# Kernel tuning notes

Hardware: AMD Instinct MI355X
Metric: run time of the kernel (lower is better)

The kernel has to match this reference:

```python
import jax, jax.numpy as jnp
import numpy as np

POS_RATIO = 0.5
EPS = 1e-6


def setup_inputs() -> dict:
    key = jax.random.key(0)
    k1, k2, k3, k4 = jax.random.split(key, 4)
    N, C, D, H, W = 8, 256, 8, 16, 16
    q = jax.random.normal(k1, (N, C, D, H, W), dtype=jnp.float32)
    k = jax.random.normal(k2, (N, C, D, H, W), dtype=jnp.float32)
    # coords: (x0, y0, z0, x1, y1, z1) with lower-right > upper-left
    uq = jax.random.uniform(k3, (N, 3), dtype=jnp.float32) * 0.5
    uk = jax.random.uniform(k4, (N, 3), dtype=jnp.float32) * 0.5
    coord_q = jnp.concatenate([uq, uq + 0.5], axis=1)
    coord_k = jnp.concatenate([uk, uk + 0.5], axis=1)
    return {"q": q, "k": k, "coord_q": coord_q, "coord_k": coord_k}


def _centers(coord, D, H, W):
    """Per-batch voxel-center coordinates. coord: [N,6]. Returns cx, cy, cz each [N, D*H*W], plus bin diag [N]."""
    bw = (coord[:, 3] - coord[:, 0]) / W  # [N]
    bh = (coord[:, 4] - coord[:, 1]) / H
    bd = (coord[:, 5] - coord[:, 2]) / D
    gz, gy, gx = jnp.meshgrid(jnp.arange(D, dtype=coord.dtype),
                              jnp.arange(H, dtype=coord.dtype),
                              jnp.arange(W, dtype=coord.dtype), indexing="ij")
    gx = (gx + 0.5).reshape(-1)[None, :]  # [1, DHW]
    gy = (gy + 0.5).reshape(-1)[None, :]
    gz = (gz + 0.5).reshape(-1)[None, :]
    cx = gx * bw[:, None] + coord[:, 0][:, None]
    cy = gy * bh[:, None] + coord[:, 1][:, None]
    cz = gz * bd[:, None] + coord[:, 2][:, None]
    diag = jnp.sqrt(bw ** 2 + bh ** 2 + bd ** 2)  # [N]
    return cx, cy, cz, diag


def reference(q, k, coord_q, coord_k):
    N, C, D, H, W = q.shape
    qf = q.reshape(N, C, -1)  # [N, C, P], P = D*H*W
    kf = k.reshape(N, C, -1)
    cqx, cqy, cqz, q_diag = _centers(coord_q, D, H, W)
    ckx, cky, ckz, k_diag = _centers(coord_k, D, H, W)
    max_diag = jnp.maximum(q_diag, k_diag)  # [N]
    # pairwise center distance, normalized by max bin diagonal: [N, P, P]
    dist = jnp.sqrt((cqx[:, :, None] - ckx[:, None, :]) ** 2
                    + (cqy[:, :, None] - cky[:, None, :]) ** 2
                    + (cqz[:, :, None] - ckz[:, None, :]) ** 2) / max_diag[:, None, None]
    pos_mask = jax.lax.stop_gradient((dist < POS_RATIO).astype(q.dtype))
    # logit[n, p, p'] = sum_c q[n,c,p] * k[n,c,p']
    logit = jnp.einsum("ncp,ncq->npq", qf, kf)
    loss = (logit * pos_mask).sum((-2, -1)) / (pos_mask.sum((-2, -1)) + EPS)  # [N]
    return -2.0 * loss.mean()
```

## Files before the change

kernel.cpp:

```cpp
#include <hip/hip_runtime.h>
#include <cstdint>
#include <cstddef>

#define NB 8
#define CH 256
#define DD 8
#define HH 16
#define WW 16
#define PP 2048

#define OFF_DPART 16384

__device__ __forceinline__ int z_window(float czq, float bdk, float k2, float maxd) {
    float lim = 0.500060f * maxd;
    int zk0 = -1;
    #pragma unroll
    for (int zk = 0; zk < DD; ++zk) {
        float czk = __fadd_rn(__fmul_rn(__fadd_rn((float)zk, 0.5f), bdk), k2);
        bool feas = fabsf(__fsub_rn(czq, czk)) < lim;
        if (feas && zk0 < 0) zk0 = zk;
    }
    if (zk0 > DD - 2) zk0 = DD - 2;
    return zk0;
}

#define CC 16
__global__ __launch_bounds__(256) void fused_kernel(
    const float* __restrict__ q, const float* __restrict__ k,
    const float* __restrict__ coord_q, const float* __restrict__ coord_k,
    float* __restrict__ partial, float* __restrict__ dpart)
{
    __shared__ float klds[CC][512];

    int t  = threadIdx.x;
    int wv = t >> 6;
    int lane = t & 63;
    int cg = blockIdx.x;
    int zq = blockIdx.y;
    int n  = blockIdx.z;
    int flat = (n * 8 + zq) * 16 + cg;
    int c0 = cg * CC;

    const float* cq = coord_q + n * 6;
    const float* ck = coord_k + n * 6;
    float q0 = cq[0], q1 = cq[1], q2 = cq[2];
    float k0 = ck[0], k1 = ck[1], k2 = ck[2];
    float bwq = __fdiv_rn(__fsub_rn(cq[3], q0), (float)WW);
    float bhq = __fdiv_rn(__fsub_rn(cq[4], q1), (float)HH);
    float bdq = __fdiv_rn(__fsub_rn(cq[5], q2), (float)DD);
    float bwk = __fdiv_rn(__fsub_rn(ck[3], k0), (float)WW);
    float bhk = __fdiv_rn(__fsub_rn(ck[4], k1), (float)HH);
    float bdk = __fdiv_rn(__fsub_rn(ck[5], k2), (float)DD);
    float diagq = __fsqrt_rn(__fadd_rn(__fadd_rn(__fmul_rn(bwq, bwq), __fmul_rn(bhq, bhq)),
                                       __fmul_rn(bdq, bdq)));
    float diagk = __fsqrt_rn(__fadd_rn(__fadd_rn(__fmul_rn(bwk, bwk), __fmul_rn(bhk, bhk)),
                                       __fmul_rn(bdk, bdk)));
    float maxd = fmaxf(diagq, diagk);
    float cqz = __fadd_rn(__fmul_rn(__fadd_rn((float)zq, 0.5f), bdq), q2);

    int zk0 = z_window(cqz, bdk, k2, maxd);
    if (zk0 < 0) {
        if (lane == 0) {
            partial[flat * 4 + wv] = 0.0f;
            if (cg == 0) dpart[(n * 8 + zq) * 4 + wv] = 0.0f;
        }
        return;
    }
    int base_p = zk0 << 8;

    int p = (zq << 8) + t;
    float qv[CC];
    {
        const float* qcol = q + ((size_t)(n * CH + c0)) * PP + p;
        #pragma unroll
        for (int c = 0; c < CC; ++c)
            qv[c] = qcol[(size_t)c * PP];
    }

    {
        const float* ksrc = k + ((size_t)(n * CH + c0)) * PP + base_p;
        #pragma unroll
        for (int i = 0; i < 8; ++i) {
            int f = i * 256 + t;
            int c = f >> 7;
            int u = (f & 127) << 2;
            float4 v = *(const float4*)(ksrc + (size_t)c * PP + u);
            klds[c][u + 0] = v.x;
            klds[c][u + 1] = v.y;
            klds[c][u + 2] = v.z;
            klds[c][u + 3] = v.w;
        }
    }
    __syncthreads();

    int ix = t & 15, iy = (t >> 4) & 15;
    float cqx = __fadd_rn(__fmul_rn(__fadd_rn((float)ix, 0.5f), bwq), q0);
    float cqy = __fadd_rn(__fmul_rn(__fadd_rn((float)iy, 0.5f), bhq), q1);

    float lim = 0.500060f * maxd;
    float tx = (cqx - k0) / bwk - 0.5f;
    float ty = (cqy - k1) / bhk - 0.5f;
    float rx = lim / bwk + 0.03f;
    float ry = lim / bhk + 0.03f;
    int jx0 = (int)ceilf(tx - rx);  if (jx0 < 0) jx0 = 0;
    int jx1 = (int)floorf(tx + rx); if (jx1 > WW - 1) jx1 = WW - 1;
    int jy0 = (int)ceilf(ty - ry);  if (jy0 < 0) jy0 = 0;
    int jy1 = (int)floorf(ty + ry); if (jy1 > HH - 1) jy1 = HH - 1;

    float half_maxd = 0.5f * maxd;
    float thr2 = half_maxd * half_maxd * 1.001f;

    float s[CC];
    #pragma unroll
    for (int c = 0; c < CC; ++c) s[c] = 0.0f;
    int cnt = 0;

    for (int dzI = 0; dzI < 2; ++dzI) {
        int jz = zk0 + dzI;
        float ckz = __fadd_rn(__fmul_rn(__fadd_rn((float)jz, 0.5f), bdk), k2);
        float dz  = __fsub_rn(cqz, ckz);
        float dz2 = __fmul_rn(dz, dz);
        for (int jy = jy0; jy <= jy1; ++jy) {
            float cky = __fadd_rn(__fmul_rn(__fadd_rn((float)jy, 0.5f), bhk), k1);
            float dy  = __fsub_rn(cqy, cky);
            float dy2 = __fmul_rn(dy, dy);
            for (int jx = jx0; jx <= jx1; ++jx) {
                float ckx = __fadd_rn(__fmul_rn(__fadd_rn((float)jx, 0.5f), bwk), k0);
                float dx  = __fsub_rn(cqx, ckx);
                float dx2 = __fmul_rn(dx, dx);
                float d2  = __fadd_rn(__fadd_rn(dx2, dy2), dz2);
                bool pos = false;
                if (d2 < thr2) {
                    float dist = __fdiv_rn(__fsqrt_rn(d2), maxd);
                    pos = dist < 0.5f;
                }
                if (pos) {
                    ++cnt;
                    int idx = (dzI << 8) + (jy << 4) + jx;
                    #pragma unroll
                    for (int c = 0; c < CC; ++c)
                        s[c] += klds[c][idx];
                }
            }
        }
    }

    float acc = 0.0f;
    #pragma unroll
    for (int c = 0; c < CC; ++c)
        acc += qv[c] * s[c];

    int ci = cnt;
    #pragma unroll
    for (int off = 32; off > 0; off >>= 1) {
        acc += __shfl_down(acc, off, 64);
        ci  += __shfl_down(ci, off, 64);
    }
    if (lane == 0) {
        partial[flat * 4 + wv] = acc;
        if (cg == 0) dpart[(n * 8 + zq) * 4 + wv] = (float)ci;
    }
}

__global__ __launch_bounds__(512) void final_kernel(const float* __restrict__ partial,
                                                    const float* __restrict__ dpart,
                                                    float* __restrict__ out)
{
    __shared__ float numsh[NB];
    __shared__ float densh[NB];
    int t = threadIdx.x;
    int n = t >> 6, lane = t & 63;

    float sp = 0.0f;
    #pragma unroll
    for (int i = 0; i < 8; ++i)
        sp += partial[n * 512 + i * 64 + lane];
    float sc = (lane < 32) ? dpart[n * 32 + lane] : 0.0f;
    #pragma unroll
    for (int off = 32; off > 0; off >>= 1) {
        sp += __shfl_down(sp, off, 64);
        sc += __shfl_down(sc, off, 64);
    }
    if (lane == 0) { numsh[n] = sp; densh[n] = sc; }
    __syncthreads();
    if (t == 0) {
        float r = 0.0f;
        for (int i = 0; i < NB; ++i)
            r += numsh[i] / (densh[i] + 1e-6f);
        out[0] = -2.0f * (r / (float)NB);
    }
}

extern "C" void kernel_launch(void* const* d_in, const int* in_sizes, int n_in,
                              void* d_out, int out_size, void* d_ws, size_t ws_size,
                              hipStream_t stream) {
    const float* q       = (const float*)d_in[0];
    const float* k       = (const float*)d_in[1];
    const float* coord_q = (const float*)d_in[2];
    const float* coord_k = (const float*)d_in[3];
    float* out = (float*)d_out;

    char* w = (char*)d_ws;
    float* partial = (float*)w;
    float* dpart   = (float*)(w + OFF_DPART);

    fused_kernel<<<dim3(CH / CC, DD, NB), 256, 0, stream>>>(q, k, coord_q, coord_k,
                                                            partial, dpart);
    final_kernel<<<1, 512, 0, stream>>>(partial, dpart, out);
}
```

Baseline: 80.39 us.

## Store K tile channel-interleaved as float4 in LDS with XOR swizzle

The shared K tile moves from [channel][voxel] scalars to float4 groups of four channels per voxel, with an XOR swizzle on the voxel index. The inner accumulation then does four 128-bit LDS reads per positive pair instead of sixteen scalar reads. The exact sqrt/divide check now runs only in a narrow band around the threshold, and the reciprocal is hoisted for the window bounds. The staging loop now transposes in registers, and the tighter threshold band relies on rounding margins holding exactly.

```diff
diff --git a/kernel.cpp b/kernel.cpp
--- a/kernel.cpp
+++ b/kernel.cpp
@@ -24,13 +24,17 @@
     return zk0;
 }
 
+__device__ __forceinline__ int lds_slot(int cq, int v) {
+    return cq * 512 + (v & ~3) + ((v & 3) ^ ((v >> 2) & 3));
+}
+
 #define CC 16
 __global__ __launch_bounds__(256) void fused_kernel(
     const float* __restrict__ q, const float* __restrict__ k,
     const float* __restrict__ coord_q, const float* __restrict__ coord_k,
     float* __restrict__ partial, float* __restrict__ dpart)
 {
-    __shared__ float klds[CC][512];
+    __shared__ float4 klds[4 * 512];
 
     int t  = threadIdx.x;
     int wv = t >> 6;
@@ -79,16 +83,22 @@
 
     {
         const float* ksrc = k + ((size_t)(n * CH + c0)) * PP + base_p;
+        int vq = t & 127;
+        int jb = t >> 7;
         #pragma unroll
-        for (int i = 0; i < 8; ++i) {
-            int f = i * 256 + t;
-            int c = f >> 7;
-            int u = (f & 127) << 2;
-            float4 v = *(const float4*)(ksrc + (size_t)c * PP + u);
-            klds[c][u + 0] = v.x;
-            klds[c][u + 1] = v.y;
-            klds[c][u + 2] = v.z;
-            klds[c][u + 3] = v.w;
+        for (int jj = 0; jj < 4; ++jj) {
+            if ((jj & 1) != jb) continue;
+            float a0[4], a1[4], a2[4], a3[4];
+            *(float4*)a0 = *(const float4*)(ksrc + (size_t)(4 * jj + 0) * PP + 4 * vq);
+            *(float4*)a1 = *(const float4*)(ksrc + (size_t)(4 * jj + 1) * PP + 4 * vq);
+            *(float4*)a2 = *(const float4*)(ksrc + (size_t)(4 * jj + 2) * PP + 4 * vq);
+            *(float4*)a3 = *(const float4*)(ksrc + (size_t)(4 * jj + 3) * PP + 4 * vq);
+            #pragma unroll
+            for (int s = 0; s < 4; ++s) {
+                float4 o;
+                o.x = a0[s]; o.y = a1[s]; o.z = a2[s]; o.w = a3[s];
+                klds[lds_slot(jj, 4 * vq + s)] = o;
+            }
         }
     }
     __syncthreads();
@@ -98,21 +108,24 @@
     float cqy = __fadd_rn(__fmul_rn(__fadd_rn((float)iy, 0.5f), bhq), q1);
 
     float lim = 0.500060f * maxd;
-    float tx = (cqx - k0) / bwk - 0.5f;
-    float ty = (cqy - k1) / bhk - 0.5f;
-    float rx = lim / bwk + 0.03f;
-    float ry = lim / bhk + 0.03f;
+    float ibwk = __frcp_rn(bwk), ibhk = __frcp_rn(bhk);
+    float tx = (cqx - k0) * ibwk - 0.5f;
+    float ty = (cqy - k1) * ibhk - 0.5f;
+    float rx = lim * ibwk + 0.031f;
+    float ry = lim * ibhk + 0.031f;
     int jx0 = (int)ceilf(tx - rx);  if (jx0 < 0) jx0 = 0;
     int jx1 = (int)floorf(tx + rx); if (jx1 > WW - 1) jx1 = WW - 1;
     int jy0 = (int)ceilf(ty - ry);  if (jy0 < 0) jy0 = 0;
     int jy1 = (int)floorf(ty + ry); if (jy1 > HH - 1) jy1 = HH - 1;
 
     float half_maxd = 0.5f * maxd;
-    float thr2 = half_maxd * half_maxd * 1.001f;
-
-    float s[CC];
-    #pragma unroll
-    for (int c = 0; c < CC; ++c) s[c] = 0.0f;
+    float T    = half_maxd * half_maxd;
+    float T_lo = T * (1.0f - 8e-7f);
+    float T_hi = T * (1.0f + 8e-7f);
+
+    float4 s4[4];
+    #pragma unroll
+    for (int c = 0; c < 4; ++c) s4[c] = make_float4(0.f, 0.f, 0.f, 0.f);
     int cnt = 0;
 
     for (int dzI = 0; dzI < 2; ++dzI) {
@@ -129,17 +142,21 @@
                 float dx  = __fsub_rn(cqx, ckx);
                 float dx2 = __fmul_rn(dx, dx);
                 float d2  = __fadd_rn(__fadd_rn(dx2, dy2), dz2);
-                bool pos = false;
-                if (d2 < thr2) {
+                bool pos = d2 < T_lo;
+                if (d2 >= T_lo && d2 < T_hi) {
                     float dist = __fdiv_rn(__fsqrt_rn(d2), maxd);
                     pos = dist < 0.5f;
                 }
                 if (pos) {
                     ++cnt;
                     int idx = (dzI << 8) + (jy << 4) + jx;
+                    int vlo = (idx & ~3) + ((idx & 3) ^ ((idx >> 2) & 3));
                     #pragma unroll
-                    for (int c = 0; c < CC; ++c)
-                        s[c] += klds[c][idx];
+                    for (int c = 0; c < 4; ++c) {
+                        float4 kv = klds[c * 512 + vlo];
+                        s4[c].x += kv.x; s4[c].y += kv.y;
+                        s4[c].z += kv.z; s4[c].w += kv.w;
+                    }
                 }
             }
         }
@@ -147,8 +164,12 @@
 
     float acc = 0.0f;
     #pragma unroll
-    for (int c = 0; c < CC; ++c)
-        acc += qv[c] * s[c];
+    for (int c = 0; c < 4; ++c) {
+        acc += qv[4 * c + 0] * s4[c].x;
+        acc += qv[4 * c + 1] * s4[c].y;
+        acc += qv[4 * c + 2] * s4[c].z;
+        acc += qv[4 * c + 3] * s4[c].w;
+    }
 
     int ci = cnt;
     #pragma unroll
```

Result: no change. 80.92 us (+0.7%).
